# Performance work log

Hardware: AMD Instinct MI355X
Metric: run time of the kernel (lower is better)

## Reference

```python
import jax, jax.numpy as jnp
import numpy as np
from jax import lax

B, C_IN, C_OUT, K, N_W, L = 32, 256, 256, 7, 8, 4096
SQ = C_IN // 32  # squeezed dim = 8
STRIDE, PAD = 1, 3


def setup_inputs() -> dict:
    key = jax.random.key(0)
    ks = jax.random.split(key, 8)
    s = 0.05
    return {
        "x": jax.random.normal(ks[0], (B, C_IN, L), dtype=jnp.float32),
        "conv_weight": jax.random.normal(ks[1], (C_OUT, C_IN, K, N_W), dtype=jnp.float32) * s,
        "w1": jax.random.normal(ks[2], (C_IN, SQ), dtype=jnp.float32) * s,   # linear1 weight (x @ w1)
        "b1": jax.random.normal(ks[3], (SQ,), dtype=jnp.float32) * s,
        "wk": jax.random.normal(ks[4], (SQ, K), dtype=jnp.float32) * s,      # kernel head
        "wi": jax.random.normal(ks[5], (SQ, C_IN), dtype=jnp.float32) * s,   # inc head
        "wo": jax.random.normal(ks[6], (SQ, C_OUT), dtype=jnp.float32) * s,  # outc head
        "wn": jax.random.normal(ks[7], (SQ, N_W), dtype=jnp.float32) * s,    # nums head
    }


def reference(x, conv_weight, w1, b1, wk, wi, wo, wn):
    # SqueezeFeedForward: AdaptiveAvgPool1d(1) == mean over length, then Linear + exact GELU
    pooled = jnp.mean(x, axis=-1)                        # [B, C_in]
    h = jax.nn.gelu(pooled @ w1 + b1, approximate=False)  # [B, SQ]

    kr = jax.nn.sigmoid(h @ wk)          # [B, K]
    inc = jax.nn.sigmoid(h @ wi)         # [B, C_in]
    outc = jax.nn.sigmoid(h @ wo)        # [B, C_out]
    nums = jax.nn.softmax(h @ wn, -1)    # [B, N_w]

    # Per-sample mixed weights: sum over num_weight of 4-way outer-product gated base weight
    w = jnp.einsum('bk,bi,bo,bn,oikn->boik', kr, inc, outc, nums, conv_weight)  # [B,O,I,K]

    b, o, i, k = w.shape
    l = x.shape[-1]
    # Batched per-sample conv via grouped conv: groups = B
    lhs = x.reshape(1, b * i, l)         # [1, B*I, L]
    rhs = w.reshape(b * o, i, k)         # [B*O, I, K]
    out = lax.conv_general_dilated(
        lhs, rhs,
        window_strides=(STRIDE,),
        padding=[(PAD, PAD)],
        dimension_numbers=('NCH', 'OIH', 'NCH'),
        feature_group_count=b,
    )
    return out.reshape(b, o, -1)         # [B, O, L_out]
```

## Files before the change

kernel.cpp:

```cpp
#include <hip/hip_runtime.h>
#include <hip/hip_bf16.h>
#include <math.h>

#define B_   32
#define CI   256
#define CO   256
#define KW   7
#define NW   8
#define SQD  8
#define L_   4096
#define PITCH 264

typedef __attribute__((ext_vector_type(8))) __bf16 bf16x8;
typedef __attribute__((ext_vector_type(4))) __bf16 bf16x4;
typedef __attribute__((ext_vector_type(4))) float  f32x4;

static __device__ __forceinline__ unsigned short f2bf(float f) {
    unsigned int u = __builtin_bit_cast(unsigned int, f);
    u += 0x7FFFu + ((u >> 16) & 1u);
    return (unsigned short)(u >> 16);
}
static __device__ __forceinline__ uint2 pack4bf(float a, float b, float c, float d) {
    bf16x4 v;
    v[0] = (__bf16)a; v[1] = (__bf16)b; v[2] = (__bf16)c; v[3] = (__bf16)d;
    return __builtin_bit_cast(uint2, v);
}

__global__ __launch_bounds__(256) void k1_mean(
        const float* __restrict__ x, float* __restrict__ pooled) {
    int row = blockIdx.x;
    const float* p = x + (size_t)row * L_;
    int t = threadIdx.x;
    float s = 0.f;
#pragma unroll
    for (int it = 0; it < 4; ++it) {
        float4 v = *(const float4*)(p + (size_t)(t + 256 * it) * 4);
        s += v.x + v.y + v.z + v.w;
    }
    for (int m = 1; m <= 32; m <<= 1) s += __shfl_xor(s, m);
    __shared__ float wsum[4];
    if ((t & 63) == 0) wsum[t >> 6] = s;
    __syncthreads();
    if (t == 0)
        pooled[row] = (wsum[0] + wsum[1] + wsum[2] + wsum[3]) * (1.0f / L_);
}

__global__ __launch_bounds__(64) void k2_gates(
        const float* __restrict__ pooled,
        const float* __restrict__ w1, const float* __restrict__ b1,
        const float* __restrict__ wk, const float* __restrict__ wi,
        const float* __restrict__ wo, const float* __restrict__ wn,
        float* __restrict__ kr, float* __restrict__ inc,
        float* __restrict__ outc, float* __restrict__ nums)
{
    int b = blockIdx.x, lane = threadIdx.x;
    float pc[4];
#pragma unroll
    for (int j = 0; j < 4; ++j)
        pc[j] = pooled[b * CI + lane + 64 * j];
    float h[SQD];
#pragma unroll
    for (int s = 0; s < SQD; ++s) {
        float ps = 0.f;
#pragma unroll
        for (int j = 0; j < 4; ++j)
            ps += pc[j] * w1[(lane + 64 * j) * SQD + s];
        for (int m = 1; m <= 32; m <<= 1) ps += __shfl_xor(ps, m);
        float z = ps + b1[s];
        h[s] = 0.5f * z * (1.0f + erff(z * 0.70710678118654752f));
    }
    if (lane < KW) {
        float a = 0.f;
#pragma unroll
        for (int s = 0; s < SQD; ++s) a += h[s] * wk[s * KW + lane];
        kr[b * 8 + lane] = 1.0f / (1.0f + expf(-a));
    }
    if (lane < NW) {
        float e[NW]; float mx = -1e30f;
#pragma unroll
        for (int n = 0; n < NW; ++n) {
            float a = 0.f;
#pragma unroll
            for (int s = 0; s < SQD; ++s) a += h[s] * wn[s * NW + n];
            e[n] = a; mx = fmaxf(mx, a);
        }
        float den = 0.f;
#pragma unroll
        for (int n = 0; n < NW; ++n) den += expf(e[n] - mx);
        nums[b * NW + lane] = expf(e[lane] - mx) / den;
    }
#pragma unroll
    for (int j = 0; j < 4; ++j) {
        int c = lane + 64 * j;
        float a = 0.f, o2 = 0.f;
#pragma unroll
        for (int s = 0; s < SQD; ++s) {
            a  += h[s] * wi[s * CI + c];
            o2 += h[s] * wo[s * CO + c];
        }
        inc[b * CI + c]  = 1.0f / (1.0f + expf(-a));
        outc[b * CO + c] = 1.0f / (1.0f + expf(-o2));
    }
}

__global__ __launch_bounds__(256) void k3_wgen(
        const float* __restrict__ cw,
        const float* __restrict__ kr, const float* __restrict__ inc,
        const float* __restrict__ outc, const float* __restrict__ nums,
        unsigned short* __restrict__ W2) {
    __shared__ float s_nums[B_][NW];
    __shared__ float s_kr[B_][KW];
    __shared__ float s_inc[B_][32];
    __shared__ float s_outc[B_][8];
    int t = threadIdx.x;
    int ic = blockIdx.x & 7, o0 = (blockIdx.x >> 3) * 8;
    s_nums[t >> 3][t & 7] = nums[t];
    if (t < B_ * KW) s_kr[t / KW][t % KW] = kr[(t / KW) * 8 + (t % KW)];
    for (int u = t; u < 32 * 32; u += 256) {
        int bb = u >> 5, ii = u & 31;
        s_inc[bb][ii] = inc[bb * CI + ic * 32 + ii];
    }
    for (int u = t; u < 32 * 8; u += 256) {
        int bb = u >> 3, oo = u & 7;
        s_outc[bb][oo] = outc[bb * CO + o0 + oo];
    }
    __syncthreads();
    int ii = t & 31, oo = t >> 5;
    int o = o0 + oo, i = ic * 32 + ii;
    float cwv[KW][NW];
    const float* p = cw + ((size_t)(o * CI + i)) * (KW * NW);
#pragma unroll
    for (int k = 0; k < KW; ++k)
#pragma unroll
        for (int n = 0; n < NW; ++n) cwv[k][n] = p[k * NW + n];
    for (int bb = 0; bb < B_; ++bb) {
        float gio = s_inc[bb][ii] * s_outc[bb][oo];
#pragma unroll
        for (int k = 0; k < KW; ++k) {
            float sk = 0.f;
#pragma unroll
            for (int n = 0; n < NW; ++n) sk += s_nums[bb][n] * cwv[k][n];
            float w = s_kr[bb][k] * gio * sk;
            W2[(((size_t)(bb * KW + k) * 8 + ic) * CO + o) * 32 + ii] = f2bf(w);
        }
    }
}

__global__ __launch_bounds__(256, 2) void k4_conv(
        const float* __restrict__ x,
        const unsigned short* __restrict__ W2,
        float* __restrict__ out) {
    __shared__ __align__(16) unsigned short xs[134 * PITCH];
    int bid = blockIdx.x;
    int wg  = (bid & 7) * 128 + (bid >> 3);
    int b = wg >> 5, l0 = (wg & 31) * 128;
    int t = threadIdx.x;
    const float* xb = x + (size_t)b * CI * L_;

    {
        int u = t >> 3;
        int lam = t & 7;
        int i0 = u * 8;
#pragma unroll
        for (int it = 0; it < 4; ++it) {
            int ch = lam + 8 * it;
            const float* src = xb + (size_t)i0 * L_ + l0 + ch * 4;
            float4 f[8];
#pragma unroll
            for (int e = 0; e < 8; ++e)
                f[e] = *(const float4*)(src + (size_t)e * L_);
#pragma unroll
            for (int j = 0; j < 4; ++j) {
                int r = ch * 4 + j + 3;
                uint2 a = pack4bf((&f[0].x)[j], (&f[1].x)[j], (&f[2].x)[j], (&f[3].x)[j]);
                uint2 c = pack4bf((&f[4].x)[j], (&f[5].x)[j], (&f[6].x)[j], (&f[7].x)[j]);
                uint4 w; w.x = a.x; w.y = a.y; w.z = c.x; w.w = c.y;
                *(uint4*)(xs + r * PITCH + u * 8) = w;
            }
        }
    }
    if (t < 192) {
        int h = t >> 5, u = t & 31;
        int r = (h < 3) ? h : (128 + h);
        int gl = l0 - 3 + r;
        bool ok = (gl >= 0 && gl < L_);
        float f[8];
#pragma unroll
        for (int e = 0; e < 8; ++e)
            f[e] = ok ? xb[(size_t)(u * 8 + e) * L_ + gl] : 0.f;
        uint2 a = pack4bf(f[0], f[1], f[2], f[3]);
        uint2 c = pack4bf(f[4], f[5], f[6], f[7]);
        uint4 w; w.x = a.x; w.y = a.y; w.z = c.x; w.w = c.y;
        *(uint4*)(xs + r * PITCH + u * 8) = w;
    }
    __syncthreads();

    int lane = t & 63, wid = t >> 6;
    int o_base = wid * 64;
    int ml = lane & 15, kg = lane >> 4;

    f32x4 acc[4][8];
#pragma unroll
    for (int a = 0; a < 4; ++a)
#pragma unroll
        for (int c = 0; c < 8; ++c) acc[a][c] = (f32x4){0.f, 0.f, 0.f, 0.f};

    const unsigned short* wA = W2 + (size_t)b * (56 * CO * 32)
                               + (o_base + ml) * 32 + kg * 8;
    const unsigned short* xB = xs + (size_t)ml * PITCH + kg * 8;

    bf16x8 afA[4], bfA[8], afB[4], bfB[8];

#pragma unroll
    for (int j = 0; j < 8; ++j)
        bfA[j] = *(const bf16x8*)(xB + (j * 16) * PITCH);
#pragma unroll
    for (int mt = 0; mt < 4; ++mt)
        afA[mt] = *(const bf16x8*)(wA + mt * 16 * 32);

    auto STEP = [&](bf16x8 (&AFc)[4], bf16x8 (&BFc)[8],
                    bf16x8 (&AFn)[4], bf16x8 (&BFn)[8],
                    int sn, bool pf) {
        int k_ = sn >> 3, icc_ = sn & 7;
#pragma unroll
        for (int j = 0; j < 8; ++j) {
            if (pf) {
                BFn[j] = *(const bf16x8*)(xB + (j * 16 + k_) * PITCH + icc_ * 32);
                if (j < 4)
                    AFn[j] = *(const bf16x8*)(wA + (size_t)sn * (CO * 32)
                                              + j * 16 * 32);
            }
#pragma unroll
            for (int mt = 0; mt < 4; ++mt)
                acc[mt][j] = __builtin_amdgcn_mfma_f32_16x16x32_bf16(
                    AFc[mt], BFc[j], acc[mt][j], 0, 0, 0);
            if (pf) {
                __builtin_amdgcn_sched_group_barrier(0x100, 1, 0);
                if (j < 4)
                    __builtin_amdgcn_sched_group_barrier(0x020, 1, 0);
            }
            __builtin_amdgcn_sched_group_barrier(0x008, 4, 0);
        }
    };

    for (int s = 0; s < 54; s += 2) {
        STEP(afA, bfA, afB, bfB, s + 1, true);
        STEP(afB, bfB, afA, bfA, s + 2, true);
    }
    STEP(afA, bfA, afB, bfB, 55, true);
    STEP(afB, bfB, afA, bfA, 0, false);

#pragma unroll
    for (int mt = 0; mt < 4; ++mt) {
        int o = o_base + mt * 16 + kg * 4;
#pragma unroll
        for (int nt = 0; nt < 8; ++nt) {
            int l = l0 + nt * 16 + ml;
            float* po = out + ((size_t)(b * CO + o)) * L_ + l;
#pragma unroll
            for (int q = 0; q < 4; ++q)
                po[(size_t)q * L_] = acc[mt][nt][q];
        }
    }
}

extern "C" void kernel_launch(void* const* d_in, const int* in_sizes, int n_in,
                              void* d_out, int out_size, void* d_ws, size_t ws_size,
                              hipStream_t stream) {
    const float* x  = (const float*)d_in[0];
    const float* cw = (const float*)d_in[1];
    const float* w1 = (const float*)d_in[2];
    const float* b1 = (const float*)d_in[3];
    const float* wk = (const float*)d_in[4];
    const float* wi = (const float*)d_in[5];
    const float* wo = (const float*)d_in[6];
    const float* wn = (const float*)d_in[7];
    float* out = (float*)d_out;

    char* ws = (char*)d_ws;
    unsigned short* W2 = (unsigned short*)(ws + 0);
    float* pooled = (float*)(ws + 29360128);
    float* kr     = (float*)(ws + 29392896);
    float* inc    = (float*)(ws + 29393920);
    float* outc   = (float*)(ws + 29426688);
    float* nums   = (float*)(ws + 29459456);

    k1_mean<<<B_ * CI, 256, 0, stream>>>(x, pooled);
    k2_gates<<<B_, 64, 0, stream>>>(pooled, w1, b1, wk, wi, wo, wn,
                                    kr, inc, outc, nums);
    k3_wgen<<<256, 256, 0, stream>>>(cw, kr, inc, outc, nums, W2);
    k4_conv<<<1024, 256, 0, stream>>>(x, W2, out);
}
```

Baseline: 166.6 us.

## Fuse gate computation into weight-generation kernel and pack two bf16 outputs

Removes the separate gate kernel: each weight-generation block now recomputes the squeeze MLP, GELU, sigmoids and softmax for all batches from the pooled means, and writes them into shared memory. Block size drops to 128 threads, and each thread handles two input channels, loading conv weights with float4 and storing two packed bf16 values per write. This saves one launch and a global round trip for the gates, at the cost of every one of the 256 blocks redoing the 256-long dot products for the hidden layer.

```diff
diff --git a/kernel.cpp b/kernel.cpp
--- a/kernel.cpp
+++ b/kernel.cpp
@@ -45,103 +45,107 @@
         pooled[row] = (wsum[0] + wsum[1] + wsum[2] + wsum[3]) * (1.0f / L_);
 }
 
-__global__ __launch_bounds__(64) void k2_gates(
+__global__ __launch_bounds__(128) void k3_wgen(
         const float* __restrict__ pooled,
         const float* __restrict__ w1, const float* __restrict__ b1,
         const float* __restrict__ wk, const float* __restrict__ wi,
         const float* __restrict__ wo, const float* __restrict__ wn,
-        float* __restrict__ kr, float* __restrict__ inc,
-        float* __restrict__ outc, float* __restrict__ nums)
-{
-    int b = blockIdx.x, lane = threadIdx.x;
-    float pc[4];
-#pragma unroll
-    for (int j = 0; j < 4; ++j)
-        pc[j] = pooled[b * CI + lane + 64 * j];
-    float h[SQD];
-#pragma unroll
-    for (int s = 0; s < SQD; ++s) {
-        float ps = 0.f;
-#pragma unroll
-        for (int j = 0; j < 4; ++j)
-            ps += pc[j] * w1[(lane + 64 * j) * SQD + s];
-        for (int m = 1; m <= 32; m <<= 1) ps += __shfl_xor(ps, m);
-        float z = ps + b1[s];
-        h[s] = 0.5f * z * (1.0f + erff(z * 0.70710678118654752f));
-    }
-    if (lane < KW) {
-        float a = 0.f;
-#pragma unroll
-        for (int s = 0; s < SQD; ++s) a += h[s] * wk[s * KW + lane];
-        kr[b * 8 + lane] = 1.0f / (1.0f + expf(-a));
-    }
-    if (lane < NW) {
-        float e[NW]; float mx = -1e30f;
-#pragma unroll
-        for (int n = 0; n < NW; ++n) {
-            float a = 0.f;
-#pragma unroll
-            for (int s = 0; s < SQD; ++s) a += h[s] * wn[s * NW + n];
-            e[n] = a; mx = fmaxf(mx, a);
-        }
-        float den = 0.f;
-#pragma unroll
-        for (int n = 0; n < NW; ++n) den += expf(e[n] - mx);
-        nums[b * NW + lane] = expf(e[lane] - mx) / den;
-    }
-#pragma unroll
-    for (int j = 0; j < 4; ++j) {
-        int c = lane + 64 * j;
-        float a = 0.f, o2 = 0.f;
-#pragma unroll
-        for (int s = 0; s < SQD; ++s) {
-            a  += h[s] * wi[s * CI + c];
-            o2 += h[s] * wo[s * CO + c];
-        }
-        inc[b * CI + c]  = 1.0f / (1.0f + expf(-a));
-        outc[b * CO + c] = 1.0f / (1.0f + expf(-o2));
-    }
-}
-
-__global__ __launch_bounds__(256) void k3_wgen(
         const float* __restrict__ cw,
-        const float* __restrict__ kr, const float* __restrict__ inc,
-        const float* __restrict__ outc, const float* __restrict__ nums,
         unsigned short* __restrict__ W2) {
+    int t  = threadIdx.x;
+    int ic = blockIdx.x & 7;
+    int o0 = (blockIdx.x >> 3) * 8;
+    __shared__ float s_h[B_][SQD];
     __shared__ float s_nums[B_][NW];
     __shared__ float s_kr[B_][KW];
     __shared__ float s_inc[B_][32];
     __shared__ float s_outc[B_][8];
-    int t = threadIdx.x;
-    int ic = blockIdx.x & 7, o0 = (blockIdx.x >> 3) * 8;
-    s_nums[t >> 3][t & 7] = nums[t];
-    if (t < B_ * KW) s_kr[t / KW][t % KW] = kr[(t / KW) * 8 + (t % KW)];
-    for (int u = t; u < 32 * 32; u += 256) {
+
+    {
+        int bb = t >> 2;
+        int s2 = (t & 3) * 2;
+#pragma unroll
+        for (int ds = 0; ds < 2; ++ds) {
+            int s = s2 + ds;
+            float ps = 0.f;
+            for (int i = 0; i < CI; ++i)
+                ps += pooled[bb * CI + i] * w1[i * SQD + s];
+            float z = ps + b1[s];
+            s_h[bb][s] = 0.5f * z * (1.0f + erff(z * 0.70710678118654752f));
+        }
+    }
+    __syncthreads();
+    if (t < B_) {
+        float e[NW], mx = -1e30f;
+#pragma unroll
+        for (int n = 0; n < NW; ++n) {
+            float a = 0.f;
+#pragma unroll
+            for (int s = 0; s < SQD; ++s) a += s_h[t][s] * wn[s * NW + n];
+            e[n] = a; mx = fmaxf(mx, a);
+        }
+        float den = 0.f;
+#pragma unroll
+        for (int n = 0; n < NW; ++n) { e[n] = expf(e[n] - mx); den += e[n]; }
+#pragma unroll
+        for (int n = 0; n < NW; ++n) s_nums[t][n] = e[n] / den;
+    }
+    for (int u = t; u < B_ * KW; u += 128) {
+        int bb = u / KW, k = u % KW;
+        float a = 0.f;
+#pragma unroll
+        for (int s = 0; s < SQD; ++s) a += s_h[bb][s] * wk[s * KW + k];
+        s_kr[bb][k] = 1.0f / (1.0f + expf(-a));
+    }
+    for (int u = t; u < B_ * 32; u += 128) {
         int bb = u >> 5, ii = u & 31;
-        s_inc[bb][ii] = inc[bb * CI + ic * 32 + ii];
-    }
-    for (int u = t; u < 32 * 8; u += 256) {
+        float a = 0.f;
+#pragma unroll
+        for (int s = 0; s < SQD; ++s) a += s_h[bb][s] * wi[s * CI + ic * 32 + ii];
+        s_inc[bb][ii] = 1.0f / (1.0f + expf(-a));
+    }
+    for (int u = t; u < B_ * 8; u += 128) {
         int bb = u >> 3, oo = u & 7;
-        s_outc[bb][oo] = outc[bb * CO + o0 + oo];
-    }
-    __syncthreads();
-    int ii = t & 31, oo = t >> 5;
-    int o = o0 + oo, i = ic * 32 + ii;
-    float cwv[KW][NW];
-    const float* p = cw + ((size_t)(o * CI + i)) * (KW * NW);
-#pragma unroll
-    for (int k = 0; k < KW; ++k)
-#pragma unroll
-        for (int n = 0; n < NW; ++n) cwv[k][n] = p[k * NW + n];
+        float a = 0.f;
+#pragma unroll
+        for (int s = 0; s < SQD; ++s) a += s_h[bb][s] * wo[s * CO + o0 + oo];
+        s_outc[bb][oo] = 1.0f / (1.0f + expf(-a));
+    }
+    __syncthreads();
+
+    int ii2 = t & 15, oo = t >> 4;
+    int o = o0 + oo;
+    int ia = ic * 32 + ii2 * 2;
+    float cwv[2][KW][NW];
+#pragma unroll
+    for (int d = 0; d < 2; ++d) {
+        const float* p = cw + ((size_t)(o * CI + ia + d)) * (KW * NW);
+#pragma unroll
+        for (int k = 0; k < KW; ++k) {
+            float4 v0 = *(const float4*)(p + k * NW);
+            float4 v1 = *(const float4*)(p + k * NW + 4);
+            cwv[d][k][0] = v0.x; cwv[d][k][1] = v0.y;
+            cwv[d][k][2] = v0.z; cwv[d][k][3] = v0.w;
+            cwv[d][k][4] = v1.x; cwv[d][k][5] = v1.y;
+            cwv[d][k][6] = v1.z; cwv[d][k][7] = v1.w;
+        }
+    }
     for (int bb = 0; bb < B_; ++bb) {
-        float gio = s_inc[bb][ii] * s_outc[bb][oo];
+        float g0 = s_inc[bb][ii2 * 2 + 0] * s_outc[bb][oo];
+        float g1 = s_inc[bb][ii2 * 2 + 1] * s_outc[bb][oo];
 #pragma unroll
         for (int k = 0; k < KW; ++k) {
-            float sk = 0.f;
-#pragma unroll
-            for (int n = 0; n < NW; ++n) sk += s_nums[bb][n] * cwv[k][n];
-            float w = s_kr[bb][k] * gio * sk;
-            W2[(((size_t)(bb * KW + k) * 8 + ic) * CO + o) * 32 + ii] = f2bf(w);
+            float sk0 = 0.f, sk1 = 0.f;
+#pragma unroll
+            for (int n = 0; n < NW; ++n) {
+                sk0 += s_nums[bb][n] * cwv[0][k][n];
+                sk1 += s_nums[bb][n] * cwv[1][k][n];
+            }
+            float krk = s_kr[bb][k];
+            unsigned int pk = (unsigned int)f2bf(krk * g0 * sk0)
+                            | ((unsigned int)f2bf(krk * g1 * sk1) << 16);
+            *(unsigned int*)(W2 + (((size_t)(bb * KW + k) * 8 + ic) * CO + o) * 32
+                             + ii2 * 2) = pk;
         }
     }
 }
@@ -280,14 +284,8 @@
     char* ws = (char*)d_ws;
     unsigned short* W2 = (unsigned short*)(ws + 0);
     float* pooled = (float*)(ws + 29360128);
-    float* kr     = (float*)(ws + 29392896);
-    float* inc    = (float*)(ws + 29393920);
-    float* outc   = (float*)(ws + 29426688);
-    float* nums   = (float*)(ws + 29459456);
 
     k1_mean<<<B_ * CI, 256, 0, stream>>>(x, pooled);
-    k2_gates<<<B_, 64, 0, stream>>>(pooled, w1, b1, wk, wi, wo, wn,
-                                    kr, inc, outc, nums);
-    k3_wgen<<<256, 256, 0, stream>>>(cw, kr, inc, outc, nums, W2);
+    k3_wgen<<<256, 128, 0, stream>>>(pooled, w1, b1, wk, wi, wo, wn, cw, W2);
     k4_conv<<<1024, 256, 0, stream>>>(x, W2, out);
 }
```

Result: slower. 183.4 us (+10.1%).
